# Optimization experiments

Measured on AMD Instinct MI355X. Metric: run time of the kernel, lower is better.

The kernel has to match this reference:

```python
import jax, jax.numpy as jnp
import numpy as np

# ---- static circuit configuration (from init_kwargs) ----
N_Q, N_L, N_A = 8, 3, 2
N_REC = N_L * N_A            # deferred-measurement record wires (measure+reset per layer/ancilla)
T = N_Q + N_A + N_REC        # 16 total wires -> 2^16 state vector
ANC = list(range(N_Q, N_Q + N_A))
C64 = jnp.complex64

# ---- constant gate matrices ----
H = (np.array([[1, 1], [1, -1]]) / np.sqrt(2)).astype(np.complex64)
SWAP = np.array([[1,0,0,0],[0,0,1,0],[0,1,0,0],[0,0,0,1]], np.complex64)
_X = np.array([[0,1],[1,0]]); _Y = np.array([[0,-1j],[1j,0]])
XX = np.kron(_X, _X).astype(np.complex64)
YY = np.kron(_Y, _Y).astype(np.complex64)
I4 = np.eye(4, dtype=np.complex64)
# doubly-controlled RX(pi/4): controls = (record wire, q1), target = q2
_th = np.pi / 4
CCRX = np.eye(8, dtype=np.complex64)
CCRX[6,6] = CCRX[7,7] = np.cos(_th/2)
CCRX[6,7] = CCRX[7,6] = -1j*np.sin(_th/2)

# ---- parameterized gate builders ----
def _rx(t):
    c = jnp.cos(t/2).astype(C64); s = (-1j*jnp.sin(t/2)).astype(C64)
    return jnp.stack([jnp.stack([c, s]), jnp.stack([s, c])])

def _ry(t):
    c = jnp.cos(t/2); s = jnp.sin(t/2)
    return jnp.stack([jnp.stack([c, -s]), jnp.stack([s, c])]).astype(C64)

def _rz(t):
    e = jnp.exp(-0.5j*t).astype(C64)
    return jnp.diag(jnp.stack([e, jnp.conj(e)]))

def _rxx(t):
    return (jnp.cos(t/2)*I4 - 1j*jnp.sin(t/2)*XX).astype(C64)

def _ryy(t):
    return (jnp.cos(t/2)*I4 - 1j*jnp.sin(t/2)*YY).astype(C64)

def _rzz(t):
    e = jnp.exp(-0.5j*t).astype(C64); f = jnp.conj(e)
    return jnp.diag(jnp.stack([e, f, f, e]))

def _crz(t):  # control first, target second
    e = jnp.exp(-0.5j*t).astype(C64); one = jnp.ones((), C64)
    return jnp.diag(jnp.stack([one, one, e, jnp.conj(e)]))

def _apply(state, U, wires):
    n = len(wires)
    U = jnp.asarray(U, C64).reshape((2,)*(2*n))
    state = jnp.tensordot(U, state, axes=(tuple(range(n, 2*n)), wires))
    return jnp.moveaxis(state, tuple(range(n)), wires)

def _simulate(x, weights, phase_weights):
    # single-sample state-vector simulation with deferred mid-circuit measurements
    state = jnp.zeros((2,)*T, C64).at[(0,)*T].set(1.0)
    for q in range(N_Q):
        state = _apply(state, H, (q,))
    rec = N_Q + N_A
    for layer in range(N_L):
        # AngleEmbedding: RY on even layers, RX on odd layers
        rot = _ry if layer % 2 == 0 else _rx
        for q in range(N_Q):
            state = _apply(state, rot(x[q]), (q,))
        # phase interference block
        pw = phase_weights[layer]
        for a in ANC:
            state = _apply(state, H, (a,))
        for i, a in enumerate(ANC):
            for j in range(N_Q):
                state = _apply(state, _crz(pw[i, j]), (j, a))
        # adaptive measurement (deferred): optional H, then swap ancilla to fresh record wire (= measure + reset)
        recs = []
        for a in ANC:
            if layer % 2 == 1:
                state = _apply(state, H, (a,))
            state = _apply(state, SWAP, (a, rec))
            recs.append(rec); rec += 1
        # parallel exchange network
        w = weights[layer]
        pairs = [(i, i+1) for i in range(0, N_Q-1, 2)]
        for i, (q1, q2) in enumerate(pairs):
            state = _apply(state, _rxx(w[3*i]), (q1, q2))
            state = _apply(state, _ryy(w[3*i+1]), (q1, q2))
            state = _apply(state, _rzz(w[3*i+2]), (q1, q2))
            if i < N_A:  # qml.cond(m_i, CRX)(pi/4) -> record-controlled CRX
                state = _apply(state, CCRX, (recs[i], q1, q2))
        off = [(i, i+1) for i in range(1, N_Q-1, 2)]
        for i, (q1, q2) in enumerate(off):
            idx = len(pairs) + i
            if 3*idx + 2 < w.shape[0]:
                state = _apply(state, _rxx(w[3*idx]), (q1, q2))
                state = _apply(state, _ryy(w[3*idx+1]), (q1, q2))
                state = _apply(state, _rzz(w[3*idx+2]), (q1, q2))
        # single-qubit variational layer on the last n_qubits*3 params
        vw = w[-N_Q*3:]
        for q in range(N_Q):
            state = _apply(state, _rx(vw[3*q]), (q,))
            state = _apply(state, _ry(vw[3*q+1]), (q,))
            state = _apply(state, _rz(vw[3*q+2]), (q,))
    # <Z_q> for the data qubits
    probs = jnp.abs(state)**2
    evs = []
    for q in range(N_Q):
        m = probs.sum(axis=tuple(a for a in range(T) if a != q))
        evs.append(m[0] - m[1])
    return jnp.stack(evs).astype(jnp.float32)


def setup_inputs() -> dict:
    key = jax.random.key(0)
    k1, k2, k3 = jax.random.split(key, 3)
    x = jax.random.normal(k1, (16, N_Q), jnp.float32)
    weights = jax.random.normal(k2, (N_L, max(N_Q*6, 24)), jnp.float32) * 0.1
    phase_weights = jax.random.normal(k3, (N_L, N_A, N_Q), jnp.float32) * 0.1
    return {"x": x, "weights": weights, "phase_weights": phase_weights}


def reference(x, weights, phase_weights):
    return jax.vmap(_simulate, in_axes=(0, None, None))(x, weights, phase_weights)
```

## Files before the change

kernel.cpp:

```cpp
#include <hip/hip_runtime.h>
#include <cstdint>


struct F2 { float x, y; };

__device__ __forceinline__ F2 cmul(F2 a, F2 b) {
  return F2{ a.x * b.x - a.y * b.y, a.x * b.y + a.y * b.x };
}
__device__ __forceinline__ F2 cfma2(F2 a, F2 b, F2 c) {
  return F2{ fmaf(a.x, b.x, fmaf(-a.y, b.y, c.x)),
             fmaf(a.x, b.y, fmaf( a.y, b.x, c.y)) };
}

template<uint32_t MASK>
__device__ __forceinline__ uint32_t pdep10(uint32_t x) {
  uint32_t r = 0;
  #pragma unroll
  for (int b = 0; b < 10; ++b) {
    if (MASK & (1u << b)) { r |= (x & 1u) << b; x >>= 1; }
  }
  return r;
}

__device__ __forceinline__ uint32_t sw(uint32_t i) { return i ^ ((i >> 5) & 31u); }

template<uint32_t MASK>
__device__ __forceinline__ void readGrp(const F2* lds, int lane, F2 a[16]) {
  const uint32_t base = pdep10<(~MASK) & 0x3FFu>((uint32_t)lane);
  #pragma unroll
  for (uint32_t j = 0; j < 16; ++j) a[j] = lds[sw(base | pdep10<MASK>(j))];
}
template<uint32_t MASK>
__device__ __forceinline__ void writeGrp(F2* lds, int lane, const F2 a[16]) {
  const uint32_t base = pdep10<(~MASK) & 0x3FFu>((uint32_t)lane);
  #pragma unroll
  for (uint32_t j = 0; j < 16; ++j) lds[sw(base | pdep10<MASK>(j))] = a[j];
}

__device__ __forceinline__ void gate1(F2 a[16], const F2 U[4], int p) {
  const int s = 1 << p;
  #pragma unroll
  for (int i = 0; i < 16; ++i) {
    if (i & s) continue;
    F2 a0 = a[i], a1 = a[i | s];
    a[i]     = cfma2(U[0], a0, cmul(U[1], a1));
    a[i | s] = cfma2(U[2], a0, cmul(U[3], a1));
  }
}

__device__ __forceinline__ void gateH(F2 a[16], int p) {
  const float R = 0.70710678118654752f;
  const int s = 1 << p;
  #pragma unroll
  for (int i = 0; i < 16; ++i) {
    if (i & s) continue;
    F2 a0 = a[i], a1 = a[i | s];
    a[i]     = F2{ (a0.x + a1.x) * R, (a0.y + a1.y) * R };
    a[i | s] = F2{ (a0.x - a1.x) * R, (a0.y - a1.y) * R };
  }
}

__device__ __forceinline__ void gateM4(F2 a[16], const F2 m[4], int p, int q) {
  const int sp = 1 << p, sq = 1 << q;
  #pragma unroll
  for (int i = 0; i < 16; ++i) {
    if (i & (sp | sq)) continue;
    F2 v0 = a[i], v1 = a[i | sq], v2 = a[i | sp], v3 = a[i | sp | sq];
    a[i]           = cfma2(m[0], v0, cmul(m[2], v3));
    a[i | sp | sq] = cfma2(m[2], v0, cmul(m[0], v3));
    a[i | sq]      = cfma2(m[1], v1, cmul(m[3], v2));
    a[i | sp]      = cfma2(m[3], v1, cmul(m[1], v2));
  }
}

__device__ __forceinline__ void gateCCRX(F2 a[16], int c1, int c2, int t) {
  const float C = 0.92387953251128674f;
  const float S = 0.38268343236508978f;
  const int cm = (1 << c1) | (1 << c2);
  const int st = 1 << t;
  #pragma unroll
  for (int i = 0; i < 16; ++i) {
    if ((i & (cm | st)) != cm) continue;
    F2 a0 = a[i], a1 = a[i | st];
    a[i]      = F2{ fmaf(C, a0.x,  S * a1.y), fmaf(C, a0.y, -S * a1.x) };
    a[i | st] = F2{ fmaf(C, a1.x,  S * a0.y), fmaf(C, a1.y, -S * a0.x) };
  }
}

__device__ __forceinline__ void rot_rx(F2 m[4], float t) {
  float c, s; __sincosf(0.5f * t, &s, &c);
  m[0] = F2{c, 0.f}; m[1] = F2{0.f, -s}; m[2] = F2{0.f, -s}; m[3] = F2{c, 0.f};
}
__device__ __forceinline__ void rot_ry(F2 m[4], float t) {
  float c, s; __sincosf(0.5f * t, &s, &c);
  m[0] = F2{c, 0.f}; m[1] = F2{-s, 0.f}; m[2] = F2{s, 0.f}; m[3] = F2{c, 0.f};
}
__device__ __forceinline__ void rot_rz(F2 m[4], float t) {
  float c, s; __sincosf(0.5f * t, &s, &c);
  m[0] = F2{c, -s}; m[1] = F2{0.f, 0.f}; m[2] = F2{0.f, 0.f}; m[3] = F2{c, s};
}
__device__ __forceinline__ void mat2mul(F2 o[4], const F2 A[4], const F2 B[4]) {
  o[0] = cfma2(A[0], B[0], cmul(A[1], B[2]));
  o[1] = cfma2(A[0], B[1], cmul(A[1], B[3]));
  o[2] = cfma2(A[2], B[0], cmul(A[3], B[2]));
  o[3] = cfma2(A[2], B[1], cmul(A[3], B[3]));
}

template<int L>
__device__ __forceinline__ void layer_tail(F2 a[16], F2* amp, int lane,
    const F2 (*M4)[4], const float* PW0, const float* PW1,
    const F2 (*Upost)[4])
{
  gateH(a, 2); gateH(a, 3);
  {
    float base0 = 0.f, base1 = 0.f;
    #pragma unroll
    for (int t = 0; t < 6; ++t) {
      const float bit = (float)((lane >> t) & 1);
      base0 += bit * PW0[2 + t];
      base1 += bit * PW1[2 + t];
    }
    const float pw00 = PW0[0], pw01 = PW0[1];
    const float pw10 = PW1[0], pw11 = PW1[1];
    #pragma unroll
    for (int dd = 0; dd < 4; ++dd) {
      const float w0 = 0.5f * (base0 + (dd & 1) * pw00 + ((dd >> 1) & 1) * pw01);
      const float w1 = 0.5f * (base1 + (dd & 1) * pw10 + ((dd >> 1) & 1) * pw11);
      float c0, s0, c1, s1;
      __sincosf(w0, &s0, &c0);
      __sincosf(w1, &s1, &c1);
      #pragma unroll
      for (int aa = 0; aa < 4; ++aa) {
        F2 f0 = F2{ c0, (aa & 1) ? s0 : -s0 };
        F2 f1 = F2{ c1, (aa & 2) ? s1 : -s1 };
        const int j = dd | (aa << 2);
        a[j] = cmul(a[j], cmul(f0, f1));
      }
    }
  }
  if (L == 1) { gateH(a, 2); gateH(a, 3); }
  gateM4(a, M4[0], 0, 1);
  gateCCRX(a, 2, 0, 1);
  writeGrp<0x303u>(amp, lane, a);
  __syncthreads();

  readGrp<0x20Eu>(amp, lane, a);
  gateM4(a, M4[1], 1, 2);
  gateCCRX(a, 3, 1, 2);
  gateM4(a, M4[4], 0, 1);
  writeGrp<0x20Eu>(amp, lane, a);
  __syncthreads();

  readGrp<0x0F0u>(amp, lane, a);
  gateM4(a, M4[2], 0, 1);
  gateM4(a, M4[3], 2, 3);
  writeGrp<0x0F0u>(amp, lane, a);
  __syncthreads();

  readGrp<0x078u>(amp, lane, a);
  gateM4(a, M4[5], 0, 1);
  gateM4(a, M4[6], 2, 3);
  if constexpr (L == 2) {
    gate1(a, Upost[3], 0); gate1(a, Upost[4], 1);
    gate1(a, Upost[5], 2); gate1(a, Upost[6], 3);
  }
  writeGrp<0x078u>(amp, lane, a);
  __syncthreads();
}

__device__ __forceinline__ void layer_head(F2 a[16], F2* amp, int lane,
                                           const F2 (*Upre)[4])
{
  gate1(a, Upre[0], 0); gate1(a, Upre[1], 1);
  gate1(a, Upre[2], 2); gate1(a, Upre[3], 3);
  writeGrp<0x00Fu>(amp, lane, a);
  __syncthreads();
  readGrp<0x0F0u>(amp, lane, a);
  gate1(a, Upre[4], 0); gate1(a, Upre[5], 1);
  gate1(a, Upre[6], 2); gate1(a, Upre[7], 3);
  writeGrp<0x0F0u>(amp, lane, a);
  __syncthreads();
  readGrp<0x303u>(amp, lane, a);
}

__device__ __forceinline__ void extract_slice(const F2* amp, int lane, int sel,
                                              F2 a[16])
{
  #pragma unroll
  for (int j = 0; j < 16; ++j) {
    const int d = j | ((lane & 15) << 4);
    F2 v = amp[sw((uint32_t)(d | (sel << 8)))];
    a[j] = (lane >> 4) ? F2{0.f, 0.f} : v;
  }
  __syncthreads();
}

__global__ __launch_bounds__(128) void zero_out_k(float* out) {
  out[threadIdx.x] = 0.f;
}

__global__ __launch_bounds__(64)
void qpie_fused(const float* __restrict__ x, const float* __restrict__ w,
                const float* __restrict__ pwg, float* __restrict__ out)
{
  __shared__ F2 amp[1024];
  __shared__ F2 sUpre[3][8][4];
  __shared__ F2 sUpost[8][4];
  __shared__ F2 sM4[3][7][4];
  __shared__ float sPW[3][2][8];

  const int lane = threadIdx.x;
  const int blk  = blockIdx.x;
  const int b  = blk >> 4;
  const int s1 = (blk >> 2) & 3;
  const int s2 = blk & 3;

  if (lane < 24) {
    const int Lp = lane >> 3, q = lane & 7;
    F2 tail[4];
    if (Lp == 0) {
      const float R = 0.70710678118654752f;
      tail[0] = F2{R, 0.f}; tail[1] = F2{R, 0.f};
      tail[2] = F2{R, 0.f}; tail[3] = F2{-R, 0.f};
    } else {
      F2 rx[4], ry[4], rz[4], t0[4];
      rot_rx(rx, w[(Lp - 1) * 48 + 24 + 3 * q]);
      rot_ry(ry, w[(Lp - 1) * 48 + 24 + 3 * q + 1]);
      rot_rz(rz, w[(Lp - 1) * 48 + 24 + 3 * q + 2]);
      mat2mul(t0, ry, rx);
      mat2mul(tail, rz, t0);
    }
    F2 rot[4];
    if ((Lp & 1) == 0) rot_ry(rot, x[b * 8 + q]); else rot_rx(rot, x[b * 8 + q]);
    F2 u[4]; mat2mul(u, rot, tail);
    #pragma unroll
    for (int k = 0; k < 4; ++k) sUpre[Lp][q][k] = u[k];
  } else if (lane < 45) {
    const int t = lane - 24;
    const int Lp = t / 7, p = t % 7;
    float cx, sx, cy, sy, cz, sz;
    __sincosf(0.5f * w[Lp * 48 + 3 * p    ], &sx, &cx);
    __sincosf(0.5f * w[Lp * 48 + 3 * p + 1], &sy, &cy);
    __sincosf(0.5f * w[Lp * 48 + 3 * p + 2], &sz, &cz);
    const F2 e  = F2{cz, -sz};
    const F2 eb = F2{cz,  sz};
    const float P = cx * cy + sx * sy, Q = cx * cy - sx * sy;
    sM4[Lp][p][0] = F2{ e.x * P,  e.y * P };
    sM4[Lp][p][1] = F2{ eb.x * Q, eb.y * Q };
    sM4[Lp][p][2] = cmul(e,  F2{0.f,  sy * cx - sx * cy});
    sM4[Lp][p][3] = cmul(eb, F2{0.f, -(sx * cy + sy * cx)});
  } else if (lane < 53) {
    const int q = lane - 45;
    F2 rx[4], ry[4], rz[4], t0[4], t1[4];
    rot_rx(rx, w[2 * 48 + 24 + 3 * q]);
    rot_ry(ry, w[2 * 48 + 24 + 3 * q + 1]);
    rot_rz(rz, w[2 * 48 + 24 + 3 * q + 2]);
    mat2mul(t0, ry, rx); mat2mul(t1, rz, t0);
    #pragma unroll
    for (int k = 0; k < 4; ++k) sUpost[q][k] = t1[k];
  } else if (lane >= 56) {
    const int k = lane - 56;
    float* pf = &sPW[0][0][0];
    #pragma unroll
    for (int m = 0; m < 6; ++m) pf[k * 6 + m] = pwg[k * 6 + m];
  }
  __syncthreads();

  F2 a[16];

  {
    F2 lf = F2{1.f, 0.f};
    #pragma unroll
    for (int t = 0; t < 6; ++t) {
      const int bit = (lane >> t) & 1;
      F2 col = bit ? sUpre[0][2 + t][2] : sUpre[0][2 + t][0];
      lf = cmul(lf, col);
    }
    F2 c01[4];
    #pragma unroll
    for (int dd = 0; dd < 4; ++dd)
      c01[dd] = cmul((dd & 1) ? sUpre[0][0][2] : sUpre[0][0][0],
                     (dd & 2) ? sUpre[0][1][2] : sUpre[0][1][0]);
    #pragma unroll
    for (int j = 0; j < 16; ++j)
      a[j] = (j >> 2) ? F2{0.f, 0.f} : cmul(lf, c01[j & 3]);
  }
  layer_tail<0>(a, amp, lane, sM4[0], sPW[0][0], sPW[0][1], sUpost);

  extract_slice(amp, lane, s1, a);
  layer_head(a, amp, lane, sUpre[1]);
  layer_tail<1>(a, amp, lane, sM4[1], sPW[1][0], sPW[1][1], sUpost);

  extract_slice(amp, lane, s2, a);
  layer_head(a, amp, lane, sUpre[2]);
  layer_tail<2>(a, amp, lane, sM4[2], sPW[2][0], sPW[2][1], sUpost);

  readGrp<0x087u>(amp, lane, a);
  gate1(a, sUpost[0], 0); gate1(a, sUpost[1], 1);
  gate1(a, sUpost[2], 2); gate1(a, sUpost[7], 3);
  float T = 0.f, E0 = 0.f, E1 = 0.f, E2 = 0.f, E7 = 0.f;
  #pragma unroll
  for (int j = 0; j < 16; ++j) {
    const float p = a[j].x * a[j].x + a[j].y * a[j].y;
    T += p;
    E0 += (j & 1) ? -p : p;
    E1 += (j & 2) ? -p : p;
    E2 += (j & 4) ? -p : p;
    E7 += (j & 8) ? -p : p;
  }
  float ev[8];
  ev[0] = E0; ev[1] = E1; ev[2] = E2; ev[7] = E7;
  ev[3] = ((lane >> 0) & 1) ? -T : T;
  ev[4] = ((lane >> 1) & 1) ? -T : T;
  ev[5] = ((lane >> 2) & 1) ? -T : T;
  ev[6] = ((lane >> 3) & 1) ? -T : T;
  #pragma unroll
  for (int q = 0; q < 8; ++q) {
    float v = ev[q];
    #pragma unroll
    for (int k = 1; k < 64; k <<= 1) v += __shfl_xor(v, k, 64);
    if (lane == 0) atomicAdd(&out[b * 8 + q], v);
  }
}

extern "C" void kernel_launch(void* const* d_in, const int* in_sizes, int n_in,
                              void* d_out, int out_size, void* d_ws, size_t ws_size,
                              hipStream_t stream) {
  (void)in_sizes; (void)n_in; (void)out_size; (void)d_ws; (void)ws_size;
  const float* x   = (const float*)d_in[0];
  const float* w   = (const float*)d_in[1];
  const float* pwg = (const float*)d_in[2];
  float* out = (float*)d_out;

  zero_out_k<<<1, 128, 0, stream>>>(out);
  qpie_fused<<<256, 64, 0, stream>>>(x, w, pwg, out);
}
```

Before: 82.27 us.

## Restructure per-layer gate schedule with ancilla ops in lanes and fewer LDS passes

Reorganizes each circuit layer so ancilla wires live in lane bits. Hadamards on the ancillas become cross-lane shuffles, and the phase gates become precomputed per-wire cos/sin diagonal factors (crz4) in place of per-lane sincos evaluation. Layer head and tail are merged and gates are reordered, which cuts the number of shared-memory transpose passes and barriers per layer. The slice extraction is folded into the first read. This trades LDS traffic and syncs for shuffles and a more complex wire-to-lane mapping, with a risk of correctness errors in the reordered gate sequence.

```diff
diff --git a/kernel.cpp b/kernel.cpp
--- a/kernel.cpp
+++ b/kernel.cpp
@@ -45,18 +45,6 @@
     F2 a0 = a[i], a1 = a[i | s];
     a[i]     = cfma2(U[0], a0, cmul(U[1], a1));
     a[i | s] = cfma2(U[2], a0, cmul(U[3], a1));
-  }
-}
-
-__device__ __forceinline__ void gateH(F2 a[16], int p) {
-  const float R = 0.70710678118654752f;
-  const int s = 1 << p;
-  #pragma unroll
-  for (int i = 0; i < 16; ++i) {
-    if (i & s) continue;
-    F2 a0 = a[i], a1 = a[i | s];
-    a[i]     = F2{ (a0.x + a1.x) * R, (a0.y + a1.y) * R };
-    a[i | s] = F2{ (a0.x - a1.x) * R, (a0.y - a1.y) * R };
   }
 }
 
@@ -73,17 +61,52 @@
   }
 }
 
-__device__ __forceinline__ void gateCCRX(F2 a[16], int c1, int c2, int t) {
+__device__ __forceinline__ void crz4(F2 a[16], const F2* CS0, const F2* CS1,
+                                     int lane) {
+  const float g0 = (lane & 16) ? 1.f : -1.f;
+  const float g1 = (lane & 32) ? 1.f : -1.f;
+  #pragma unroll
+  for (int t = 0; t < 4; ++t) {
+    const F2 c0 = CS0[t], c1 = CS1[t];
+    const F2 g = cmul(F2{c0.x, g0 * c0.y}, F2{c1.x, g1 * c1.y});
+    #pragma unroll
+    for (int j = 0; j < 16; ++j)
+      if (j & (1 << t)) a[j] = cmul(a[j], g);
+  }
+}
+
+__device__ __forceinline__ void hAnc(F2 a[16], int bit, int lane) {
+  const float R = 0.70710678118654752f;
+  const float s = (lane & bit) ? -1.f : 1.f;
+  #pragma unroll
+  for (int j = 0; j < 16; ++j) {
+    const float px = __shfl_xor(a[j].x, bit, 64);
+    const float py = __shfl_xor(a[j].y, bit, 64);
+    a[j].x = fmaf(s, a[j].x, px) * R;
+    a[j].y = fmaf(s, a[j].y, py) * R;
+  }
+}
+
+__device__ __forceinline__ void ccrx2(F2 a[16], int lane) {
   const float C = 0.92387953251128674f;
   const float S = 0.38268343236508978f;
-  const int cm = (1 << c1) | (1 << c2);
-  const int st = 1 << t;
-  #pragma unroll
-  for (int i = 0; i < 16; ++i) {
-    if ((i & (cm | st)) != cm) continue;
-    F2 a0 = a[i], a1 = a[i | st];
-    a[i]      = F2{ fmaf(C, a0.x,  S * a1.y), fmaf(C, a0.y, -S * a1.x) };
-    a[i | st] = F2{ fmaf(C, a1.x,  S * a0.y), fmaf(C, a1.y, -S * a0.x) };
+  if (lane & 16) {
+    #pragma unroll
+    for (int i = 0; i < 16; ++i) {
+      if ((i & 3) != 1) continue;
+      F2 a0 = a[i], a1 = a[i | 2];
+      a[i]     = F2{ fmaf(C, a0.x,  S * a1.y), fmaf(C, a0.y, -S * a1.x) };
+      a[i | 2] = F2{ fmaf(C, a1.x,  S * a0.y), fmaf(C, a1.y, -S * a0.x) };
+    }
+  }
+  if (lane & 32) {
+    #pragma unroll
+    for (int i = 0; i < 16; ++i) {
+      if ((i & 12) != 4) continue;
+      F2 a0 = a[i], a1 = a[i | 8];
+      a[i]     = F2{ fmaf(C, a0.x,  S * a1.y), fmaf(C, a0.y, -S * a1.x) };
+      a[i | 8] = F2{ fmaf(C, a1.x,  S * a0.y), fmaf(C, a1.y, -S * a0.x) };
+    }
   }
 }
 
@@ -107,91 +130,46 @@
 }
 
 template<int L>
-__device__ __forceinline__ void layer_tail(F2 a[16], F2* amp, int lane,
-    const F2 (*M4)[4], const float* PW0, const float* PW1,
+__device__ __forceinline__ void do_layer(F2 a[16], F2* amp, int lane, int sel,
+    const F2 (*Upre)[4], const F2 (*M4)[4], const F2* CS0, const F2* CS1,
     const F2 (*Upost)[4])
 {
-  gateH(a, 2); gateH(a, 3);
-  {
-    float base0 = 0.f, base1 = 0.f;
-    #pragma unroll
-    for (int t = 0; t < 6; ++t) {
-      const float bit = (float)((lane >> t) & 1);
-      base0 += bit * PW0[2 + t];
-      base1 += bit * PW1[2 + t];
-    }
-    const float pw00 = PW0[0], pw01 = PW0[1];
-    const float pw10 = PW1[0], pw11 = PW1[1];
-    #pragma unroll
-    for (int dd = 0; dd < 4; ++dd) {
-      const float w0 = 0.5f * (base0 + (dd & 1) * pw00 + ((dd >> 1) & 1) * pw01);
-      const float w1 = 0.5f * (base1 + (dd & 1) * pw10 + ((dd >> 1) & 1) * pw11);
-      float c0, s0, c1, s1;
-      __sincosf(w0, &s0, &c0);
-      __sincosf(w1, &s1, &c1);
-      #pragma unroll
-      for (int aa = 0; aa < 4; ++aa) {
-        F2 f0 = F2{ c0, (aa & 1) ? s0 : -s0 };
-        F2 f1 = F2{ c1, (aa & 2) ? s1 : -s1 };
-        const int j = dd | (aa << 2);
-        a[j] = cmul(a[j], cmul(f0, f1));
-      }
-    }
-  }
-  if (L == 1) { gateH(a, 2); gateH(a, 3); }
-  gateM4(a, M4[0], 0, 1);
-  gateCCRX(a, 2, 0, 1);
-  writeGrp<0x303u>(amp, lane, a);
-  __syncthreads();
-
-  readGrp<0x20Eu>(amp, lane, a);
-  gateM4(a, M4[1], 1, 2);
-  gateCCRX(a, 3, 1, 2);
-  gateM4(a, M4[4], 0, 1);
-  writeGrp<0x20Eu>(amp, lane, a);
-  __syncthreads();
-
-  readGrp<0x0F0u>(amp, lane, a);
+  if constexpr (L > 0) {
+    #pragma unroll
+    for (int j = 0; j < 16; ++j)
+      a[j] = amp[sw((uint32_t)((lane & 15) | (j << 4) | (sel << 8)))];
+    __syncthreads();
+    gate1(a, Upre[4], 0); gate1(a, Upre[5], 1);
+    gate1(a, Upre[6], 2); gate1(a, Upre[7], 3);
+  }
+  crz4(a, CS0 + 4, CS1 + 4, lane);
   gateM4(a, M4[2], 0, 1);
   gateM4(a, M4[3], 2, 3);
+  gateM4(a, M4[6], 1, 2);
   writeGrp<0x0F0u>(amp, lane, a);
   __syncthreads();
 
-  readGrp<0x078u>(amp, lane, a);
-  gateM4(a, M4[5], 0, 1);
-  gateM4(a, M4[6], 2, 3);
-  if constexpr (L == 2) {
-    gate1(a, Upost[3], 0); gate1(a, Upost[4], 1);
-    gate1(a, Upost[5], 2); gate1(a, Upost[6], 3);
-  }
-  writeGrp<0x078u>(amp, lane, a);
-  __syncthreads();
-}
-
-__device__ __forceinline__ void layer_head(F2 a[16], F2* amp, int lane,
-                                           const F2 (*Upre)[4])
-{
-  gate1(a, Upre[0], 0); gate1(a, Upre[1], 1);
-  gate1(a, Upre[2], 2); gate1(a, Upre[3], 3);
+  readGrp<0x00Fu>(amp, lane, a);
+  if constexpr (L > 0) {
+    gate1(a, Upre[0], 0); gate1(a, Upre[1], 1);
+    gate1(a, Upre[2], 2); gate1(a, Upre[3], 3);
+  }
+  crz4(a, CS0, CS1, lane);
+  gateM4(a, M4[0], 0, 1);
+  gateM4(a, M4[1], 2, 3);
+  if constexpr (L == 1) { hAnc(a, 16, lane); hAnc(a, 32, lane); }
+  ccrx2(a, lane);
+  gateM4(a, M4[4], 1, 2);
   writeGrp<0x00Fu>(amp, lane, a);
   __syncthreads();
-  readGrp<0x0F0u>(amp, lane, a);
-  gate1(a, Upre[4], 0); gate1(a, Upre[5], 1);
-  gate1(a, Upre[6], 2); gate1(a, Upre[7], 3);
-  writeGrp<0x0F0u>(amp, lane, a);
-  __syncthreads();
-  readGrp<0x303u>(amp, lane, a);
-}
-
-__device__ __forceinline__ void extract_slice(const F2* amp, int lane, int sel,
-                                              F2 a[16])
-{
-  #pragma unroll
-  for (int j = 0; j < 16; ++j) {
-    const int d = j | ((lane & 15) << 4);
-    F2 v = amp[sw((uint32_t)(d | (sel << 8)))];
-    a[j] = (lane >> 4) ? F2{0.f, 0.f} : v;
-  }
+
+  readGrp<0x03Cu>(amp, lane, a);
+  gateM4(a, M4[5], 1, 2);
+  if constexpr (L == 2) {
+    gate1(a, Upost[2], 0); gate1(a, Upost[3], 1);
+    gate1(a, Upost[4], 2); gate1(a, Upost[5], 3);
+  }
+  writeGrp<0x03Cu>(amp, lane, a);
   __syncthreads();
 }
 
@@ -207,7 +185,7 @@
   __shared__ F2 sUpre[3][8][4];
   __shared__ F2 sUpost[8][4];
   __shared__ F2 sM4[3][7][4];
-  __shared__ float sPW[3][2][8];
+  __shared__ F2 sCS[3][2][8];
 
   const int lane = threadIdx.x;
   const int blk  = blockIdx.x;
@@ -233,6 +211,10 @@
     F2 rot[4];
     if ((Lp & 1) == 0) rot_ry(rot, x[b * 8 + q]); else rot_rx(rot, x[b * 8 + q]);
     F2 u[4]; mat2mul(u, rot, tail);
+    if (q == 4) {
+      #pragma unroll
+      for (int k = 0; k < 4; ++k) { u[k].x *= 0.5f; u[k].y *= 0.5f; }
+    }
     #pragma unroll
     for (int k = 0; k < 4; ++k) sUpre[Lp][q][k] = u[k];
   } else if (lane < 45) {
@@ -258,62 +240,56 @@
     mat2mul(t0, ry, rx); mat2mul(t1, rz, t0);
     #pragma unroll
     for (int k = 0; k < 4; ++k) sUpost[q][k] = t1[k];
-  } else if (lane >= 56) {
-    const int k = lane - 56;
-    float* pf = &sPW[0][0][0];
-    #pragma unroll
-    for (int m = 0; m < 6; ++m) pf[k * 6 + m] = pwg[k * 6 + m];
+  }
+  if (lane < 48) {
+    const float v = pwg[lane];
+    float c, s; __sincosf(0.5f * v, &s, &c);
+    (&sCS[0][0][0])[lane] = F2{c, s};
   }
   __syncthreads();
 
   F2 a[16];
 
   {
-    F2 lf = F2{1.f, 0.f};
-    #pragma unroll
-    for (int t = 0; t < 6; ++t) {
-      const int bit = (lane >> t) & 1;
-      F2 col = bit ? sUpre[0][2 + t][2] : sUpre[0][2 + t][0];
-      lf = cmul(lf, col);
-    }
-    F2 c01[4];
-    #pragma unroll
-    for (int dd = 0; dd < 4; ++dd)
-      c01[dd] = cmul((dd & 1) ? sUpre[0][0][2] : sUpre[0][0][0],
-                     (dd & 2) ? sUpre[0][1][2] : sUpre[0][1][0]);
+    F2 lf = (lane & 1) ? sUpre[0][0][2] : sUpre[0][0][0];
+    #pragma unroll
+    for (int t = 1; t < 4; ++t)
+      lf = cmul(lf, ((lane >> t) & 1) ? sUpre[0][t][2] : sUpre[0][t][0]);
+    F2 c45[4], c67[4];
+    #pragma unroll
+    for (int k = 0; k < 4; ++k) {
+      c45[k] = cmul((k & 1) ? sUpre[0][4][2] : sUpre[0][4][0],
+                    (k & 2) ? sUpre[0][5][2] : sUpre[0][5][0]);
+      c67[k] = cmul((k & 1) ? sUpre[0][6][2] : sUpre[0][6][0],
+                    (k & 2) ? sUpre[0][7][2] : sUpre[0][7][0]);
+    }
     #pragma unroll
     for (int j = 0; j < 16; ++j)
-      a[j] = (j >> 2) ? F2{0.f, 0.f} : cmul(lf, c01[j & 3]);
-  }
-  layer_tail<0>(a, amp, lane, sM4[0], sPW[0][0], sPW[0][1], sUpost);
-
-  extract_slice(amp, lane, s1, a);
-  layer_head(a, amp, lane, sUpre[1]);
-  layer_tail<1>(a, amp, lane, sM4[1], sPW[1][0], sPW[1][1], sUpost);
-
-  extract_slice(amp, lane, s2, a);
-  layer_head(a, amp, lane, sUpre[2]);
-  layer_tail<2>(a, amp, lane, sM4[2], sPW[2][0], sPW[2][1], sUpost);
-
-  readGrp<0x087u>(amp, lane, a);
+      a[j] = cmul(lf, cmul(c45[j & 3], c67[j >> 2]));
+  }
+  do_layer<0>(a, amp, lane, 0,  sUpre[0], sM4[0], sCS[0][0], sCS[0][1], sUpost);
+  do_layer<1>(a, amp, lane, s1, sUpre[1], sM4[1], sCS[1][0], sCS[1][1], sUpost);
+  do_layer<2>(a, amp, lane, s2, sUpre[2], sM4[2], sCS[2][0], sCS[2][1], sUpost);
+
+  readGrp<0x0C3u>(amp, lane, a);
   gate1(a, sUpost[0], 0); gate1(a, sUpost[1], 1);
-  gate1(a, sUpost[2], 2); gate1(a, sUpost[7], 3);
-  float T = 0.f, E0 = 0.f, E1 = 0.f, E2 = 0.f, E7 = 0.f;
+  gate1(a, sUpost[6], 2); gate1(a, sUpost[7], 3);
+  float T = 0.f, E0 = 0.f, E1 = 0.f, E6 = 0.f, E7 = 0.f;
   #pragma unroll
   for (int j = 0; j < 16; ++j) {
     const float p = a[j].x * a[j].x + a[j].y * a[j].y;
     T += p;
     E0 += (j & 1) ? -p : p;
     E1 += (j & 2) ? -p : p;
-    E2 += (j & 4) ? -p : p;
+    E6 += (j & 4) ? -p : p;
     E7 += (j & 8) ? -p : p;
   }
   float ev[8];
-  ev[0] = E0; ev[1] = E1; ev[2] = E2; ev[7] = E7;
-  ev[3] = ((lane >> 0) & 1) ? -T : T;
-  ev[4] = ((lane >> 1) & 1) ? -T : T;
-  ev[5] = ((lane >> 2) & 1) ? -T : T;
-  ev[6] = ((lane >> 3) & 1) ? -T : T;
+  ev[0] = E0; ev[1] = E1; ev[6] = E6; ev[7] = E7;
+  ev[2] = (lane & 1) ? -T : T;
+  ev[3] = (lane & 2) ? -T : T;
+  ev[4] = (lane & 4) ? -T : T;
+  ev[5] = (lane & 8) ? -T : T;
   #pragma unroll
   for (int q = 0; q < 8; ++q) {
     float v = ev[q];
```

After: 82.01 us. About the same (-0.3%).
